# Kernel optimization log

Hardware: AMD Instinct MI355X
Metric: run time of the kernel (lower is better)

Reference implementation:

```python
import jax, jax.numpy as jnp
import numpy as np

N_KPS = 1024      # number of TPS control points
N_PTS = 120000    # number of query points to warp
RELAX = 0.5       # TPS relaxation (regularization on K diagonal)


def setup_inputs() -> dict:
    key = jax.random.key(0)
    k1, k2, k3 = jax.random.split(key, 3)
    # Control points in a [0,100)^2 coordinate frame.
    kps_a = jax.random.uniform(k1, (N_KPS, 2), dtype=jnp.float32) * 100.0
    kps_b = kps_a + jax.random.normal(k2, (N_KPS, 2), dtype=jnp.float32) * 2.0
    # --- replicate __init__: solve the TPS system for W ---
    d2 = jnp.sum((kps_a[:, None, :] - kps_a[None, :, :]) ** 2, axis=-1)  # [n_a, n_a]
    d2 = jnp.where(d2 == 0, 1.0, d2)
    K = 0.5 * d2 * jnp.log(d2) + RELAX * jnp.eye(N_KPS, dtype=jnp.float32)
    P = jnp.concatenate([jnp.ones((N_KPS, 1), jnp.float32), kps_a], axis=1)  # [n_a, 3]
    L = jnp.block([[K, P], [P.T, jnp.zeros((3, 3), jnp.float32)]])           # [n_a+3, n_a+3]
    v = jnp.concatenate([kps_b - kps_a, jnp.zeros((3, 2), jnp.float32)], axis=0)
    W = jnp.linalg.solve(L, v)  # [n_a+3, 2]  (equivalent to L.inverse() @ v)
    # Query points
    pts = jax.random.uniform(k3, (N_PTS, 2), dtype=jnp.float32) * 100.0
    return {"pts": pts, "kps_a": kps_a, "W": W}


def reference(pts, kps_a, W):
    # pairwise squared distances, [n_a, n_b] (matches __build_l2_mat)
    l2 = jnp.sum((kps_a[:, None, :] - pts[None, :, :]) ** 2, axis=-1)
    l2 = jnp.where(l2 == 0, 1.0, l2)
    v = 0.5 * l2 * jnp.log(l2)  # TPS radial basis r^2 * log(r)
    ones = jnp.ones_like(pts[:, 0])
    affine = jnp.stack([ones, pts[:, 0], pts[:, 1]], axis=0)   # [3, n_b]
    x = jnp.concatenate([v, affine], axis=0)                   # [n_a+3, n_b]
    z = x.T @ W                                                # [n_b, 2]
    return pts + z
```

## Files before the change

kernel.cpp:

```cpp
#include <hip/hip_runtime.h>

#define N_KPS 1024
#define N_PTS 120000
#define BLOCK 512
#define KSPLIT 8
#define KCHUNK (N_KPS / KSPLIT)
#define PTS_PER_BLOCK 128
#define CHUNK 8
#define NCHUNK (KCHUNK / CHUNK)

typedef float v2f __attribute__((ext_vector_type(2)));

__global__ __launch_bounds__(BLOCK) void tps_warp_kernel(
    const float2* __restrict__ pts,
    const float*  __restrict__ kps,
    const float*  __restrict__ W,
    float2*       __restrict__ out)
{
    __shared__ float4 part[KSPLIT][64];

    const int lane = threadIdx.x & 63;
    const int wv = __builtin_amdgcn_readfirstlane(threadIdx.x) >> 6;

    const int base = blockIdx.x * PTS_PER_BLOCK;
    const int j0 = base + lane;
    const int j1 = base + 64 + lane;
    const int j0c = j0 < N_PTS ? j0 : N_PTS - 1;
    const int j1c = j1 < N_PTS ? j1 : N_PTS - 1;
    const float2 p0 = pts[j0c];
    const float2 p1 = pts[j1c];

    v2f px = {p0.x, p1.x};
    v2f py = {p0.y, p1.y};
    v2f zx = {0.0f, 0.0f};
    v2f zy = {0.0f, 0.0f};
    const v2f tiny = {1e-37f, 1e-37f};

    auto eval = [&](float kx, float ky, float wx, float wy) {
        v2f dx = v2f{kx, kx} - px;
        v2f dy = v2f{ky, ky} - py;
        v2f d2 = __builtin_elementwise_fma(
            dy, dy, __builtin_elementwise_fma(dx, dx, tiny));
        v2f t;
        t.x = __log2f(d2.x);
        t.y = __log2f(d2.y);
        v2f v = d2 * t;
        zx = __builtin_elementwise_fma(v, v2f{wx, wx}, zx);
        zy = __builtin_elementwise_fma(v, v2f{wy, wy}, zy);
    };

    const float4* __restrict__ kp4 = (const float4*)kps;
    const float4* __restrict__ wp4 = (const float4*)W;
    const int cbase = wv * (KCHUNK / 2);

    #pragma unroll
    for (int c = 0; c < NCHUNK; ++c) {
        float4 kc[4], wc[4];
        #pragma unroll
        for (int t = 0; t < 4; ++t) {
            kc[t] = kp4[cbase + c * 4 + t];
            wc[t] = wp4[cbase + c * 4 + t];
        }
        #pragma unroll
        for (int t = 0; t < 4; ++t) {
            eval(kc[t].x, kc[t].y, wc[t].x, wc[t].y);
            eval(kc[t].z, kc[t].w, wc[t].z, wc[t].w);
        }
    }

    part[wv][lane] = make_float4(zx.x, zy.x, zx.y, zy.y);
    __syncthreads();

    if (wv < 2) {
        const bool hi = (wv == 1);
        const float2 p = hi ? p1 : p0;
        const int j = hi ? j1 : j0;

        float sx = 0.f, sy = 0.f;
        #pragma unroll
        for (int w = 0; w < KSPLIT; w += 2) {
            float4 a = part[w][lane];
            float4 b = part[w + 1][lane];
            sx += (hi ? a.z : a.x) + (hi ? b.z : b.x);
            sy += (hi ? a.w : a.y) + (hi ? b.w : b.y);
        }

        const float scale = 0.34657359027997264f;
        float w1x = W[2048], w1y = W[2049];
        float wxx = W[2050], wxy = W[2051];
        float wyx = W[2052], wyy = W[2053];

        if (j < N_PTS) {
            float ox = p.x + fmaf(scale, sx, fmaf(wxx, p.x, fmaf(wyx, p.y, w1x)));
            float oy = p.y + fmaf(scale, sy, fmaf(wxy, p.x, fmaf(wyy, p.y, w1y)));
            out[j] = make_float2(ox, oy);
        }
    }
}

extern "C" void kernel_launch(void* const* d_in, const int* in_sizes, int n_in,
                              void* d_out, int out_size, void* d_ws, size_t ws_size,
                              hipStream_t stream) {
    const float* pts = (const float*)d_in[0];
    const float* kps = (const float*)d_in[1];
    const float* W   = (const float*)d_in[2];
    float* out = (float*)d_out;

    const int grid = (N_PTS + PTS_PER_BLOCK - 1) / PTS_PER_BLOCK;
    tps_warp_kernel<<<grid, BLOCK, 0, stream>>>(
        (const float2*)pts, kps, W, (float2*)out);
}
```

Before: 78.32 us.

## Stage control points in LDS and process three points per lane

Each block now copies all control points and their weights into shared memory as packed float4 entries. Each lane then evaluates three query points per control point read from LDS, replacing the global float4 loads and packed two-point math. This amortises each control-point fetch over more points and reduces the block count. The cost is per-block staging work, an extra barrier, and the loss of explicit packed arithmetic, and it assumes the point count divides the block size exactly.

```diff
diff --git a/kernel.cpp b/kernel.cpp
--- a/kernel.cpp
+++ b/kernel.cpp
@@ -5,11 +5,10 @@
 #define BLOCK 512
 #define KSPLIT 8
 #define KCHUNK (N_KPS / KSPLIT)
-#define PTS_PER_BLOCK 128
-#define CHUNK 8
-#define NCHUNK (KCHUNK / CHUNK)
+#define PTS_PER_LANE 3
+#define PTS_PER_BLOCK 192
 
-typedef float v2f __attribute__((ext_vector_type(2)));
+typedef float v4f __attribute__((ext_vector_type(4)));
 
 __global__ __launch_bounds__(BLOCK) void tps_warp_kernel(
     const float2* __restrict__ pts,
@@ -17,84 +16,95 @@
     const float*  __restrict__ W,
     float2*       __restrict__ out)
 {
-    __shared__ float4 part[KSPLIT][64];
+    __shared__ v4f ctrl[N_KPS];
+    __shared__ float2 part[PTS_PER_LANE][KSPLIT][64];
 
-    const int lane = threadIdx.x & 63;
-    const int wv = __builtin_amdgcn_readfirstlane(threadIdx.x) >> 6;
+    const int tid = threadIdx.x;
+    const int lane = tid & 63;
+    const int wv = __builtin_amdgcn_readfirstlane(tid) >> 6;
 
-    const int base = blockIdx.x * PTS_PER_BLOCK;
-    const int j0 = base + lane;
-    const int j1 = base + 64 + lane;
-    const int j0c = j0 < N_PTS ? j0 : N_PTS - 1;
-    const int j1c = j1 < N_PTS ? j1 : N_PTS - 1;
-    const float2 p0 = pts[j0c];
-    const float2 p1 = pts[j1c];
-
-    v2f px = {p0.x, p1.x};
-    v2f py = {p0.y, p1.y};
-    v2f zx = {0.0f, 0.0f};
-    v2f zy = {0.0f, 0.0f};
-    const v2f tiny = {1e-37f, 1e-37f};
-
-    auto eval = [&](float kx, float ky, float wx, float wy) {
-        v2f dx = v2f{kx, kx} - px;
-        v2f dy = v2f{ky, ky} - py;
-        v2f d2 = __builtin_elementwise_fma(
-            dy, dy, __builtin_elementwise_fma(dx, dx, tiny));
-        v2f t;
-        t.x = __log2f(d2.x);
-        t.y = __log2f(d2.y);
-        v2f v = d2 * t;
-        zx = __builtin_elementwise_fma(v, v2f{wx, wx}, zx);
-        zy = __builtin_elementwise_fma(v, v2f{wy, wy}, zy);
-    };
-
-    const float4* __restrict__ kp4 = (const float4*)kps;
-    const float4* __restrict__ wp4 = (const float4*)W;
-    const int cbase = wv * (KCHUNK / 2);
-
-    #pragma unroll
-    for (int c = 0; c < NCHUNK; ++c) {
-        float4 kc[4], wc[4];
+    {
+        const float2* kp2 = (const float2*)kps;
+        const float2* wp2 = (const float2*)W;
         #pragma unroll
-        for (int t = 0; t < 4; ++t) {
-            kc[t] = kp4[cbase + c * 4 + t];
-            wc[t] = wp4[cbase + c * 4 + t];
-        }
-        #pragma unroll
-        for (int t = 0; t < 4; ++t) {
-            eval(kc[t].x, kc[t].y, wc[t].x, wc[t].y);
-            eval(kc[t].z, kc[t].w, wc[t].z, wc[t].w);
+        for (int i = tid; i < N_KPS; i += BLOCK) {
+            float2 k = kp2[i];
+            float2 w = wp2[i];
+            ctrl[i] = v4f{k.x, k.y, w.x, w.y};
         }
     }
 
-    part[wv][lane] = make_float4(zx.x, zy.x, zx.y, zy.y);
+    const int base = blockIdx.x * PTS_PER_BLOCK;
+    float px0, py0, px1, py1, px2, py2;
+    {
+        float2 p0 = pts[base + 0 * 64 + lane];
+        float2 p1 = pts[base + 1 * 64 + lane];
+        float2 p2 = pts[base + 2 * 64 + lane];
+        px0 = p0.x; py0 = p0.y;
+        px1 = p1.x; py1 = p1.y;
+        px2 = p2.x; py2 = p2.y;
+    }
+
     __syncthreads();
 
-    if (wv < 2) {
-        const bool hi = (wv == 1);
-        const float2 p = hi ? p1 : p0;
-        const int j = hi ? j1 : j0;
+    float ax0 = 0.f, ay0 = 0.f;
+    float ax1 = 0.f, ay1 = 0.f;
+    float ax2 = 0.f, ay2 = 0.f;
 
+    const int c0 = wv * KCHUNK;
+    #pragma unroll 8
+    for (int i = 0; i < KCHUNK; ++i) {
+        v4f c = ctrl[c0 + i];
+        const float kx = c.x, ky = c.y, wx = c.z, wy = c.w;
+        {
+            float dx = kx - px0, dy = ky - py0;
+            float d2 = fmaf(dy, dy, fmaf(dx, dx, 1e-37f));
+            float v = d2 * __log2f(d2);
+            ax0 = fmaf(v, wx, ax0);
+            ay0 = fmaf(v, wy, ay0);
+        }
+        {
+            float dx = kx - px1, dy = ky - py1;
+            float d2 = fmaf(dy, dy, fmaf(dx, dx, 1e-37f));
+            float v = d2 * __log2f(d2);
+            ax1 = fmaf(v, wx, ax1);
+            ay1 = fmaf(v, wy, ay1);
+        }
+        {
+            float dx = kx - px2, dy = ky - py2;
+            float d2 = fmaf(dy, dy, fmaf(dx, dx, 1e-37f));
+            float v = d2 * __log2f(d2);
+            ax2 = fmaf(v, wx, ax2);
+            ay2 = fmaf(v, wy, ay2);
+        }
+    }
+
+    part[0][wv][lane] = make_float2(ax0, ay0);
+    part[1][wv][lane] = make_float2(ax1, ay1);
+    part[2][wv][lane] = make_float2(ax2, ay2);
+    __syncthreads();
+
+    if (wv < PTS_PER_LANE) {
+        const int s = wv;
         float sx = 0.f, sy = 0.f;
         #pragma unroll
-        for (int w = 0; w < KSPLIT; w += 2) {
-            float4 a = part[w][lane];
-            float4 b = part[w + 1][lane];
-            sx += (hi ? a.z : a.x) + (hi ? b.z : b.x);
-            sy += (hi ? a.w : a.y) + (hi ? b.w : b.y);
+        for (int w = 0; w < KSPLIT; ++w) {
+            float2 a = part[s][w][lane];
+            sx += a.x;
+            sy += a.y;
         }
+
+        const float qx = (s == 0) ? px0 : (s == 1) ? px1 : px2;
+        const float qy = (s == 0) ? py0 : (s == 1) ? py1 : py2;
 
         const float scale = 0.34657359027997264f;
         float w1x = W[2048], w1y = W[2049];
         float wxx = W[2050], wxy = W[2051];
         float wyx = W[2052], wyy = W[2053];
 
-        if (j < N_PTS) {
-            float ox = p.x + fmaf(scale, sx, fmaf(wxx, p.x, fmaf(wyx, p.y, w1x)));
-            float oy = p.y + fmaf(scale, sy, fmaf(wxy, p.x, fmaf(wyy, p.y, w1y)));
-            out[j] = make_float2(ox, oy);
-        }
+        float ox = qx + fmaf(scale, sx, fmaf(wxx, qx, fmaf(wyx, qy, w1x)));
+        float oy = qy + fmaf(scale, sy, fmaf(wxy, qx, fmaf(wyy, qy, w1y)));
+        out[base + s * 64 + lane] = make_float2(ox, oy);
     }
 }
 
@@ -106,7 +116,7 @@
     const float* W   = (const float*)d_in[2];
     float* out = (float*)d_out;
 
-    const int grid = (N_PTS + PTS_PER_BLOCK - 1) / PTS_PER_BLOCK;
+    const int grid = N_PTS / PTS_PER_BLOCK;
     tps_warp_kernel<<<grid, BLOCK, 0, stream>>>(
         (const float2*)pts, kps, W, (float2*)out);
 }
```

New measurement: 88.32 us. 1.13x slower.
